# Kernel optimization log

Hardware: AMD Instinct MI355X
Metric: run time of the kernel (lower is better)

The kernel has to match this reference:

```python
import jax, jax.numpy as jnp
import numpy as np

N = 50000
E = 800000
IN_DIM = 512
H1 = IN_DIM // 2   # 256
H2 = IN_DIM // 4   # 128
D = 8
NP_CAYLEY = D * (D - 1) // 2  # 28


def setup_inputs() -> dict:
    key = jax.random.key(0)
    ks = jax.random.split(key, 10)
    x = jax.random.normal(ks[0], (N, IN_DIM), dtype=jnp.float32)
    edge_index = jax.random.randint(ks[1], (2, E), 0, N, dtype=jnp.int64)
    s1 = 1.0 / np.sqrt(IN_DIM)
    s2 = 1.0 / np.sqrt(H1)
    s3 = 1.0 / np.sqrt(H2)
    W1l = jax.random.uniform(ks[2], (H1, IN_DIM), jnp.float32, -s1, s1)
    b1 = jax.random.uniform(ks[3], (H1,), jnp.float32, -s1, s1)
    W1r = jax.random.uniform(ks[4], (H1, IN_DIM), jnp.float32, -s1, s1)
    W2l = jax.random.uniform(ks[5], (H2, H1), jnp.float32, -s2, s2)
    b2 = jax.random.uniform(ks[6], (H2,), jnp.float32, -s2, s2)
    W2r = jax.random.uniform(ks[7], (H2, H1), jnp.float32, -s2, s2)
    Wp = jax.random.uniform(ks[8], (NP_CAYLEY, H2), jnp.float32, -s3, s3)
    bp = jax.random.uniform(ks[9], (NP_CAYLEY,), jnp.float32, -s3, s3)
    return {"x": x, "edge_index": edge_index,
            "W1l": W1l, "b1": b1, "W1r": W1r,
            "W2l": W2l, "b2": b2, "W2r": W2r,
            "Wp": Wp, "bp": bp}


def _sage_conv(x, src, dst, Wl, bl, Wr):
    # PyG SAGEConv (mean aggr): out = lin_l(mean_{j in N(i)} x_j) + lin_r(x_i)
    msg_sum = jax.ops.segment_sum(x[src], dst, num_segments=N)  # [N, F]
    deg = jax.ops.segment_sum(jnp.ones((src.shape[0],), x.dtype), dst,
                              num_segments=N)
    mean = msg_sum / jnp.maximum(deg, 1.0)[:, None]
    return mean @ Wl.T + bl + x @ Wr.T


def _cayley(params):
    # params: [N, d(d-1)/2] -> skew A, then O = (I - A)^{-1} (I + A)
    iu, ju = jnp.triu_indices(D, k=1)  # row-major i<j matches torch loop order
    n = params.shape[0]
    A = jnp.zeros((n, D, D), params.dtype)
    A = A.at[:, iu, ju].set(params)
    A = A.at[:, ju, iu].set(-params)
    I = jnp.eye(D, dtype=params.dtype)
    return jnp.linalg.solve(I[None] - A, I[None] + A)


def reference(x, edge_index, W1l, b1, W1r, W2l, b2, W2r, Wp, bp):
    src, dst = edge_index[0], edge_index[1]
    h = jax.nn.relu(_sage_conv(x, src, dst, W1l, b1, W1r))
    h = jax.nn.relu(_sage_conv(h, src, dst, W2l, b2, W2r))
    params = h @ Wp.T + bp  # [N, 28]
    return _cayley(params)  # [N, 8, 8]
```

## Files before the change

### kernel.cpp

```cpp
#include <hip/hip_runtime.h>
#include <hip/hip_bf16.h>


#define WS_ALIGN(x) (((x) + 255) & ~size_t(255))

typedef __attribute__((ext_vector_type(8))) short short8;
typedef __attribute__((ext_vector_type(4))) float floatx4;

static __device__ __forceinline__ ushort f2b(float f) {
    unsigned u = __builtin_bit_cast(unsigned, f);
    u = (u + 0x7fffu + ((u >> 16) & 1u)) >> 16;
    return (ushort)u;
}
static __device__ __forceinline__ float b2f(ushort h) {
    unsigned u = ((unsigned)h) << 16;
    return __builtin_bit_cast(float, u);
}
static __device__ __forceinline__ unsigned pk2(float a, float b) {
    return (unsigned)f2b(a) | ((unsigned)f2b(b) << 16);
}


__global__ __launch_bounds__(256)
void prep_kernel(const int* __restrict__ dst, int* __restrict__ deg, int E, int eb,
                 const float* __restrict__ W1l, const float* __restrict__ W1r,
                 const float* __restrict__ W2l, const float* __restrict__ W2r,
                 ushort* __restrict__ Wc1, ushort* __restrict__ Wc2) {
    const int b = blockIdx.x;
    const int tid = threadIdx.x;
    if (b < eb) {
        int e = b * 256 + tid;
        if (e < E) atomicAdd(&deg[dst[e]], 1);
    } else {
        int idx = (b - eb) * 256 + tid;
        const int n1 = (512 * 512) / 8;
        const int n2 = (256 * 256) / 8;
        const float* src;
        ushort* dstp;
        if (idx < n1) {
            int e = idx * 8;
            int row = e >> 9, col = e & 511;
            src = (row < 256) ? &W1l[row * 512 + col] : &W1r[(row - 256) * 512 + col];
            dstp = &Wc1[e];
        } else if (idx < n1 + n2) {
            int e = (idx - n1) * 8;
            int row = e >> 8, col = e & 255;
            src = (row < 128) ? &W2l[row * 256 + col] : &W2r[(row - 128) * 256 + col];
            dstp = &Wc2[e];
        } else {
            return;
        }
        const float4* s4 = reinterpret_cast<const float4*>(src);
        float4 v0 = s4[0], v1 = s4[1];
        short8 o;
        o[0] = (short)f2b(v0.x); o[1] = (short)f2b(v0.y);
        o[2] = (short)f2b(v0.z); o[3] = (short)f2b(v0.w);
        o[4] = (short)f2b(v1.x); o[5] = (short)f2b(v1.y);
        o[6] = (short)f2b(v1.z); o[7] = (short)f2b(v1.w);
        *reinterpret_cast<short8*>(dstp) = o;
    }
}


__global__ __launch_bounds__(256)
void scan_phase1(const int* __restrict__ deg, int* __restrict__ bsum, int n) {
    __shared__ int red[256];
    const int t = threadIdx.x;
    const int i = blockIdx.x * 1024 + t * 4;
    int s = 0;
    if (i + 4 <= n) {
        int4 v = *reinterpret_cast<const int4*>(&deg[i]);
        s = v.x + v.y + v.z + v.w;
    } else {
        for (int k = i; k < n; ++k) s += deg[k];
    }
    red[t] = s;
    __syncthreads();
#pragma unroll
    for (int off = 128; off > 0; off >>= 1) {
        if (t < off) red[t] += red[t + off];
        __syncthreads();
    }
    if (t == 0) bsum[blockIdx.x] = red[0];
}

__global__ __launch_bounds__(256)
void scan_phase2(int* __restrict__ bsum, int* __restrict__ rowptr, int nb, int n) {
    __shared__ int sh[256];
    const int t = threadIdx.x;
    int orig = (t < nb) ? bsum[t] : 0;
    sh[t] = orig;
    __syncthreads();
#pragma unroll
    for (int off = 1; off < 256; off <<= 1) {
        int v = (t >= off) ? sh[t - off] : 0;
        __syncthreads();
        sh[t] += v;
        __syncthreads();
    }
    if (t < nb) bsum[t] = sh[t] - orig;
    if (t == 255) rowptr[n] = sh[255];
}

__global__ __launch_bounds__(256)
void scan_phase3(const int* __restrict__ deg, const int* __restrict__ bsum,
                 int* __restrict__ rowptr, int* __restrict__ cursor, int n) {
    __shared__ int red[256];
    const int t = threadIdx.x;
    const int i = blockIdx.x * 1024 + t * 4;
    int v0 = 0, v1 = 0, v2 = 0, v3 = 0;
    if (i + 4 <= n) {
        int4 v = *reinterpret_cast<const int4*>(&deg[i]);
        v0 = v.x; v1 = v.y; v2 = v.z; v3 = v.w;
    } else {
        if (i     < n) v0 = deg[i];
        if (i + 1 < n) v1 = deg[i + 1];
        if (i + 2 < n) v2 = deg[i + 2];
        if (i + 3 < n) v3 = deg[i + 3];
    }
    int s = v0 + v1 + v2 + v3;
    red[t] = s;
    __syncthreads();
#pragma unroll
    for (int off = 1; off < 256; off <<= 1) {
        int u = (t >= off) ? red[t - off] : 0;
        __syncthreads();
        red[t] += u;
        __syncthreads();
    }
    int pre = bsum[blockIdx.x] + red[t] - s;
    if (i + 4 <= n) {
        int4 o;
        o.x = pre; o.y = pre + v0; o.z = pre + v0 + v1; o.w = pre + v0 + v1 + v2;
        *reinterpret_cast<int4*>(&rowptr[i]) = o;
        *reinterpret_cast<int4*>(&cursor[i]) = make_int4(0, 0, 0, 0);
    } else {
        if (i     < n) { rowptr[i]     = pre;                cursor[i]     = 0; }
        if (i + 1 < n) { rowptr[i + 1] = pre + v0;           cursor[i + 1] = 0; }
        if (i + 2 < n) { rowptr[i + 2] = pre + v0 + v1;      cursor[i + 2] = 0; }
        if (i + 3 < n) { rowptr[i + 3] = pre + v0 + v1 + v2; cursor[i + 3] = 0; }
    }
}

__global__ void scatter_kernel(const int* __restrict__ src, const int* __restrict__ dst,
                               const int* __restrict__ rowptr, int* __restrict__ cursor,
                               int* __restrict__ adj, int E) {
    int e = blockIdx.x * blockDim.x + threadIdx.x;
    if (e < E) {
        int d = dst[e];
        int p = atomicAdd(&cursor[d], 1);
        adj[rowptr[d] + p] = src[e];
    }
}


template <bool CASTA>
__global__ __launch_bounds__(512, 4)
void gemm_wide(const float* __restrict__ Af, const ushort* __restrict__ Ab,
               const ushort* __restrict__ B,
               ushort* __restrict__ Cl, ushort* __restrict__ Cr,
               int M, int K, int Ncols, int S) {
    __shared__ ushort As[128 * 64];
    __shared__ ushort Bs[256 * 64];
    const int tid  = threadIdx.x;
    const int wave = tid >> 6;
    const int lane = tid & 63;
    const int row0 = blockIdx.y * 128;
    const int col0 = blockIdx.x * 256;
    const int wm = (wave & 1) * 64;
    const int wn = (wave >> 1) * 64;

    floatx4 acc[4][4];
#pragma unroll
    for (int i = 0; i < 4; ++i)
#pragma unroll
        for (int j = 0; j < 4; ++j)
            acc[i][j] = (floatx4){0.f, 0.f, 0.f, 0.f};

    const int rsub = lane >> 3;
    const int ksw  = ((lane & 7) * 16) ^ (rsub << 4);

    const int ar = tid >> 2;
    const int aq = tid & 3;
    int agrow = row0 + ar; if (agrow >= M) agrow = M - 1;
    const float* arow_base = CASTA ? (Af + (size_t)agrow * K + aq * 16) : nullptr;
    char* alds = (char*)As + ar * 128;
    const int arx = (ar & 7) << 4;

    float4 va0, va1, va2, va3;
    if constexpr (CASTA) {
        const float* s0 = arow_base;
        va0 = *reinterpret_cast<const float4*>(s0 + 0);
        va1 = *reinterpret_cast<const float4*>(s0 + 4);
        va2 = *reinterpret_cast<const float4*>(s0 + 8);
        va3 = *reinterpret_cast<const float4*>(s0 + 12);
    }

    for (int k0 = 0; k0 < K; k0 += 64) {
#pragma unroll
        for (int i = 0; i < 4; ++i) {
            int chunk = wave * 4 + i;
            int r = chunk * 8 + rsub;
            int gcol = col0 + r;
            const char* src = (const char*)(B + (size_t)gcol * K + k0) + ksw;
            __builtin_amdgcn_global_load_lds(
                (const __attribute__((address_space(1))) unsigned int*)src,
                (__attribute__((address_space(3))) unsigned int*)(&Bs[chunk * 512]),
                16, 0, 0);
        }
        if constexpr (CASTA) {
            uint4 o0 = make_uint4(pk2(va0.x, va0.y), pk2(va0.z, va0.w),
                                  pk2(va1.x, va1.y), pk2(va1.z, va1.w));
            uint4 o1 = make_uint4(pk2(va2.x, va2.y), pk2(va2.z, va2.w),
                                  pk2(va3.x, va3.y), pk2(va3.z, va3.w));
            int g0 = aq * 2;
            *reinterpret_cast<uint4*>(alds + ((g0 * 16) ^ arx))       = o0;
            *reinterpret_cast<uint4*>(alds + (((g0 + 1) * 16) ^ arx)) = o1;
            if (k0 + 64 < K) {
                const float* s1 = arow_base + k0 + 64;
                va0 = *reinterpret_cast<const float4*>(s1 + 0);
                va1 = *reinterpret_cast<const float4*>(s1 + 4);
                va2 = *reinterpret_cast<const float4*>(s1 + 8);
                va3 = *reinterpret_cast<const float4*>(s1 + 12);
            }
        } else {
#pragma unroll
            for (int i = 0; i < 2; ++i) {
                int chunk = wave * 2 + i;
                int r = chunk * 8 + rsub;
                int grow = row0 + r;
                if (grow >= M) grow = M - 1;
                const char* src = (const char*)(Ab + (size_t)grow * K + k0) + ksw;
                __builtin_amdgcn_global_load_lds(
                    (const __attribute__((address_space(1))) unsigned int*)src,
                    (__attribute__((address_space(3))) unsigned int*)(&As[chunk * 512]),
                    16, 0, 0);
            }
        }
        __syncthreads();

#pragma unroll
        for (int kk = 0; kk < 2; ++kk) {
            short8 af[4], bf[4];
            const int kb = (kk * 64 + ((lane >> 4) << 4)) ^ ((lane & 7) << 4);
#pragma unroll
            for (int im = 0; im < 4; ++im) {
                int r = wm + im * 16 + (lane & 15);
                af[im] = *reinterpret_cast<const short8*>((const char*)As + r * 128 + kb);
            }
#pragma unroll
            for (int in = 0; in < 4; ++in) {
                int r = wn + in * 16 + (lane & 15);
                bf[in] = *reinterpret_cast<const short8*>((const char*)Bs + r * 128 + kb);
            }
#pragma unroll
            for (int im = 0; im < 4; ++im)
#pragma unroll
                for (int in = 0; in < 4; ++in)
                    acc[im][in] = __builtin_amdgcn_mfma_f32_16x16x32_bf16(
                        af[im], bf[in], acc[im][in], 0, 0, 0);
        }
        __syncthreads();
    }

#pragma unroll
    for (int im = 0; im < 4; ++im) {
#pragma unroll
        for (int reg = 0; reg < 4; ++reg) {
            int r = row0 + wm + im * 16 + ((lane >> 4) << 2) + reg;
            if (r < M) {
#pragma unroll
                for (int in = 0; in < 4; ++in) {
                    int g = col0 + wn + in * 16 + (lane & 15);
                    if (g < S) Cl[(size_t)r * S + g] = f2b(acc[im][in][reg]);
                    else       Cr[(size_t)r * S + (g - S)] = f2b(acc[im][in][reg]);
                }
            }
        }
    }
}


template <int LPN>
__global__ __launch_bounds__(256)
void aggregate_bf16(const ushort* __restrict__ Yl, const ushort* __restrict__ Yr,
                    const float* __restrict__ bias,
                    const int* __restrict__ rowptr, const int* __restrict__ adj,
                    ushort* __restrict__ H, int n) {
    constexpr int F = LPN * 8;
    const int grp = threadIdx.x / LPN;
    const int sub = threadIdx.x % LPN;
    const int node = blockIdx.x * (256 / LPN) + grp;
    if (node >= n) return;
    const int c = sub * 8;
    const int start = rowptr[node], end = rowptr[node + 1];

    float acc[8];
#pragma unroll
    for (int v = 0; v < 8; ++v) acc[v] = 0.f;

    int e = start;
    for (; e + 4 <= end; e += 4) {
        int s0 = adj[e + 0], s1 = adj[e + 1], s2 = adj[e + 2], s3 = adj[e + 3];
        short8 r0 = *reinterpret_cast<const short8*>(&Yl[(size_t)s0 * F + c]);
        short8 r1 = *reinterpret_cast<const short8*>(&Yl[(size_t)s1 * F + c]);
        short8 r2 = *reinterpret_cast<const short8*>(&Yl[(size_t)s2 * F + c]);
        short8 r3 = *reinterpret_cast<const short8*>(&Yl[(size_t)s3 * F + c]);
#pragma unroll
        for (int v = 0; v < 8; ++v)
            acc[v] += (b2f((ushort)r0[v]) + b2f((ushort)r1[v])) +
                      (b2f((ushort)r2[v]) + b2f((ushort)r3[v]));
    }
    for (; e < end; ++e) {
        int s = adj[e];
        short8 r = *reinterpret_cast<const short8*>(&Yl[(size_t)s * F + c]);
#pragma unroll
        for (int v = 0; v < 8; ++v) acc[v] += b2f((ushort)r[v]);
    }

    const int d = end - start;
    const float inv = 1.0f / (float)(d > 0 ? d : 1);
    short8 sv = *reinterpret_cast<const short8*>(&Yr[(size_t)node * F + c]);
    float4 bv0 = *reinterpret_cast<const float4*>(&bias[c]);
    float4 bv1 = *reinterpret_cast<const float4*>(&bias[c + 4]);
    float bb[8] = {bv0.x, bv0.y, bv0.z, bv0.w, bv1.x, bv1.y, bv1.z, bv1.w};
    short8 o;
#pragma unroll
    for (int v = 0; v < 8; ++v)
        o[v] = (short)f2b(fmaxf(acc[v] * inv + b2f((ushort)sv[v]) + bb[v], 0.f));
    *reinterpret_cast<short8*>(&H[(size_t)node * F + c]) = o;
}


__global__ __launch_bounds__(256)
void params_kernel(const ushort* __restrict__ H2, const float* __restrict__ Wp,
                   const float* __restrict__ bp, float* __restrict__ P, int n) {
    __shared__ float WpS[32 * 132];
    __shared__ float bpS[32];
    for (int t = threadIdx.x; t < 32 * 132; t += 256) WpS[t] = 0.f;
    if (threadIdx.x < 32) bpS[threadIdx.x] = (threadIdx.x < 28) ? bp[threadIdx.x] : 0.f;
    __syncthreads();
    for (int t = threadIdx.x; t < 28 * 128; t += 256) {
        int r = t >> 7, c = t & 127;
        WpS[r * 132 + c] = Wp[t];
    }
    __syncthreads();

    const int node = blockIdx.x * 32 + (threadIdx.x >> 3);
    const int l = threadIdx.x & 7;
    if (node >= n) return;

    short8 h8[16];
    const short8* hp = reinterpret_cast<const short8*>(&H2[(size_t)node * 128]);
#pragma unroll
    for (int q = 0; q < 16; ++q) h8[q] = hp[q];

    float acc0 = bpS[l], acc1 = bpS[l + 8], acc2 = bpS[l + 16], acc3 = bpS[l + 24];
#pragma unroll
    for (int q = 0; q < 32; ++q) {
        float h0 = b2f((ushort)h8[q >> 1][(q & 1) * 4 + 0]);
        float h1 = b2f((ushort)h8[q >> 1][(q & 1) * 4 + 1]);
        float h2 = b2f((ushort)h8[q >> 1][(q & 1) * 4 + 2]);
        float h3 = b2f((ushort)h8[q >> 1][(q & 1) * 4 + 3]);
        float4 w0 = *reinterpret_cast<const float4*>(&WpS[(l +  0) * 132 + 4 * q]);
        float4 w1 = *reinterpret_cast<const float4*>(&WpS[(l +  8) * 132 + 4 * q]);
        float4 w2 = *reinterpret_cast<const float4*>(&WpS[(l + 16) * 132 + 4 * q]);
        float4 w3 = *reinterpret_cast<const float4*>(&WpS[(l + 24) * 132 + 4 * q]);
        acc0 += h0 * w0.x + h1 * w0.y + h2 * w0.z + h3 * w0.w;
        acc1 += h0 * w1.x + h1 * w1.y + h2 * w1.z + h3 * w1.w;
        acc2 += h0 * w2.x + h1 * w2.y + h2 * w2.z + h3 * w2.w;
        acc3 += h0 * w3.x + h1 * w3.y + h2 * w3.z + h3 * w3.w;
    }
    float* pout = &P[(size_t)node * 32];
    pout[l]      = acc0;
    pout[l + 8]  = acc1;
    pout[l + 16] = acc2;
    pout[l + 24] = acc3;
}


__global__ __launch_bounds__(256)
void cayley_kernel(const float* __restrict__ P, float* __restrict__ Out, int n) {
    int i = blockIdx.x * blockDim.x + threadIdx.x;
    if (i >= n) return;
    float p[28];
    const float4* pp = reinterpret_cast<const float4*>(&P[(size_t)i * 32]);
#pragma unroll
    for (int q = 0; q < 7; ++q) {
        float4 v = pp[q];
        p[4 * q + 0] = v.x; p[4 * q + 1] = v.y;
        p[4 * q + 2] = v.z; p[4 * q + 3] = v.w;
    }

    float M_[8][8], B_[8][8];
#pragma unroll
    for (int r = 0; r < 8; ++r)
#pragma unroll
        for (int c = 0; c < 8; ++c) {
            M_[r][c] = (r == c) ? 1.f : 0.f;
            B_[r][c] = (r == c) ? 1.f : 0.f;
        }
    {
        int idx = 0;
#pragma unroll
        for (int r = 0; r < 8; ++r)
#pragma unroll
            for (int c = r + 1; c < 8; ++c) {
                float a = p[idx++];
                M_[r][c] -= a;  M_[c][r] += a;
                B_[r][c] += a;  B_[c][r] -= a;
            }
    }
#pragma unroll
    for (int col = 0; col < 8; ++col) {
        float inv = 1.0f / M_[col][col];
#pragma unroll
        for (int c = 0; c < 8; ++c) { M_[col][c] *= inv; B_[col][c] *= inv; }
#pragma unroll
        for (int r = 0; r < 8; ++r) {
            if (r == col) continue;
            float f = M_[r][col];
#pragma unroll
            for (int c = 0; c < 8; ++c) {
                M_[r][c] -= f * M_[col][c];
                B_[r][c] -= f * B_[col][c];
            }
        }
    }
    float* out = &Out[(size_t)i * 64];
#pragma unroll
    for (int r = 0; r < 8; ++r) {
        float4 o0 = make_float4(B_[r][0], B_[r][1], B_[r][2], B_[r][3]);
        float4 o1 = make_float4(B_[r][4], B_[r][5], B_[r][6], B_[r][7]);
        *reinterpret_cast<float4*>(&out[r * 8 + 0]) = o0;
        *reinterpret_cast<float4*>(&out[r * 8 + 4]) = o1;
    }
}


extern "C" void kernel_launch(void* const* d_in, const int* in_sizes, int n_in,
                              void* d_out, int out_size, void* d_ws, size_t ws_size,
                              hipStream_t stream) {
    const float* x   = (const float*)d_in[0];
    const int*   ei  = (const int*)d_in[1];
    const float* W1l = (const float*)d_in[2];
    const float* b1  = (const float*)d_in[3];
    const float* W1r = (const float*)d_in[4];
    const float* W2l = (const float*)d_in[5];
    const float* b2  = (const float*)d_in[6];
    const float* W2r = (const float*)d_in[7];
    const float* Wp  = (const float*)d_in[8];
    const float* bp  = (const float*)d_in[9];
    float* out = (float*)d_out;

    const int IN_DIM = 512;
    const int N = in_sizes[0] / IN_DIM;
    const int E = in_sizes[1] / 2;

    char* ws = (char*)d_ws;
    size_t off = 0;
    int* deg      = (int*)(ws + off); off = WS_ALIGN(off + (size_t)N * 4);
    int* rowptr   = (int*)(ws + off); off = WS_ALIGN(off + (size_t)(N + 1) * 4);
    int* cursor   = (int*)(ws + off); off = WS_ALIGN(off + (size_t)N * 4);
    int* bsum     = (int*)(ws + off); off = WS_ALIGN(off + (size_t)256 * 4);
    int* adj      = (int*)(ws + off); off = WS_ALIGN(off + (size_t)E * 4);
    ushort* Yl    = (ushort*)(ws + off); off = WS_ALIGN(off + (size_t)N * 256 * 2);
    ushort* Yr    = (ushort*)(ws + off); off = WS_ALIGN(off + (size_t)N * 256 * 2);
    ushort* h1    = (ushort*)(ws + off); off = WS_ALIGN(off + (size_t)N * 256 * 2);
    ushort* zl    = (ushort*)(ws + off); off = WS_ALIGN(off + (size_t)N * 128 * 2);
    ushort* zr    = (ushort*)(ws + off); off = WS_ALIGN(off + (size_t)N * 128 * 2);
    ushort* Wc1   = (ushort*)(ws + off); off = WS_ALIGN(off + (size_t)512 * 512 * 2);
    ushort* Wc2   = (ushort*)(ws + off); off = WS_ALIGN(off + (size_t)256 * 256 * 2);
    float*  Pp    = (float*)(ws + off);  off = WS_ALIGN(off + (size_t)N * 32 * 4);

    const int* src = ei;
    const int* dst = ei + E;

    hipMemsetAsync(deg, 0, (size_t)N * 4, stream);

    const int eb = (E + 255) / 256;
    const int wb = ((512 * 512 + 256 * 256) / 8 + 255) / 256;
    const int nb = (N + 1023) / 1024;

    prep_kernel<<<eb + wb, 256, 0, stream>>>(
        dst, deg, E, eb, W1l, W1r, W2l, W2r, Wc1, Wc2);
    scan_phase1<<<nb, 256, 0, stream>>>(deg, bsum, N);
    scan_phase2<<<1, 256, 0, stream>>>(bsum, rowptr, nb, N);
    scan_phase3<<<nb, 256, 0, stream>>>(deg, bsum, rowptr, cursor, N);
    scatter_kernel<<<eb, 256, 0, stream>>>(src, dst, rowptr, cursor, adj, E);

    int gm = (N + 127) / 128;

    gemm_wide<true><<<dim3(2, gm), 512, 0, stream>>>(
        x, (const ushort*)nullptr, Wc1, Yl, Yr, N, 512, 512, 256);
    aggregate_bf16<32><<<(N + 7) / 8, 256, 0, stream>>>(Yl, Yr, b1, rowptr, adj, h1, N);

    gemm_wide<false><<<dim3(1, gm), 512, 0, stream>>>(
        (const float*)nullptr, h1, Wc2, zl, zr, N, 256, 256, 128);
    ushort* h2 = Yl;
    aggregate_bf16<16><<<(N + 15) / 16, 256, 0, stream>>>(zl, zr, b2, rowptr, adj, h2, N);

    params_kernel<<<(N + 31) / 32, 256, 0, stream>>>(h2, Wp, bp, Pp, N);
    cayley_kernel<<<(N + 255) / 256, 256, 0, stream>>>(Pp, out, N);
}
```

Measured before the change: 276.6 us.

## Fuse degree histogram into first GEMM, fuse params with Cayley, split second GEMM

```diff
diff --git a/kernel.cpp b/kernel.cpp
--- a/kernel.cpp
+++ b/kernel.cpp
@@ -22,43 +22,35 @@
 
 
 __global__ __launch_bounds__(256)
-void prep_kernel(const int* __restrict__ dst, int* __restrict__ deg, int E, int eb,
-                 const float* __restrict__ W1l, const float* __restrict__ W1r,
+void prep_kernel(const float* __restrict__ W1l, const float* __restrict__ W1r,
                  const float* __restrict__ W2l, const float* __restrict__ W2r,
                  ushort* __restrict__ Wc1, ushort* __restrict__ Wc2) {
-    const int b = blockIdx.x;
-    const int tid = threadIdx.x;
-    if (b < eb) {
-        int e = b * 256 + tid;
-        if (e < E) atomicAdd(&deg[dst[e]], 1);
+    int idx = blockIdx.x * blockDim.x + threadIdx.x;
+    const int n1 = (512 * 512) / 8;
+    const int n2 = (256 * 256) / 8;
+    const float* src;
+    ushort* dstp;
+    if (idx < n1) {
+        int e = idx * 8;
+        int row = e >> 9, col = e & 511;
+        src = (row < 256) ? &W1l[row * 512 + col] : &W1r[(row - 256) * 512 + col];
+        dstp = &Wc1[e];
+    } else if (idx < n1 + n2) {
+        int e = (idx - n1) * 8;
+        int row = e >> 8, col = e & 255;
+        src = (row < 128) ? &W2l[row * 256 + col] : &W2r[(row - 128) * 256 + col];
+        dstp = &Wc2[e];
     } else {
-        int idx = (b - eb) * 256 + tid;
-        const int n1 = (512 * 512) / 8;
-        const int n2 = (256 * 256) / 8;
-        const float* src;
-        ushort* dstp;
-        if (idx < n1) {
-            int e = idx * 8;
-            int row = e >> 9, col = e & 511;
-            src = (row < 256) ? &W1l[row * 512 + col] : &W1r[(row - 256) * 512 + col];
-            dstp = &Wc1[e];
-        } else if (idx < n1 + n2) {
-            int e = (idx - n1) * 8;
-            int row = e >> 8, col = e & 255;
-            src = (row < 128) ? &W2l[row * 256 + col] : &W2r[(row - 128) * 256 + col];
-            dstp = &Wc2[e];
-        } else {
-            return;
-        }
-        const float4* s4 = reinterpret_cast<const float4*>(src);
-        float4 v0 = s4[0], v1 = s4[1];
-        short8 o;
-        o[0] = (short)f2b(v0.x); o[1] = (short)f2b(v0.y);
-        o[2] = (short)f2b(v0.z); o[3] = (short)f2b(v0.w);
-        o[4] = (short)f2b(v1.x); o[5] = (short)f2b(v1.y);
-        o[6] = (short)f2b(v1.z); o[7] = (short)f2b(v1.w);
-        *reinterpret_cast<short8*>(dstp) = o;
-    }
+        return;
+    }
+    const float4* s4 = reinterpret_cast<const float4*>(src);
+    float4 v0 = s4[0], v1 = s4[1];
+    short8 o;
+    o[0] = (short)f2b(v0.x); o[1] = (short)f2b(v0.y);
+    o[2] = (short)f2b(v0.z); o[3] = (short)f2b(v0.w);
+    o[4] = (short)f2b(v1.x); o[5] = (short)f2b(v1.y);
+    o[6] = (short)f2b(v1.z); o[7] = (short)f2b(v1.w);
+    *reinterpret_cast<short8*>(dstp) = o;
 }
 
 
@@ -154,27 +146,37 @@
 }
 
 
-template <bool CASTA>
-__global__ __launch_bounds__(512, 4)
+template <bool CASTA, int BN, bool HIST>
+__global__ __launch_bounds__(512, 6)
 void gemm_wide(const float* __restrict__ Af, const ushort* __restrict__ Ab,
                const ushort* __restrict__ B,
                ushort* __restrict__ Cl, ushort* __restrict__ Cr,
-               int M, int K, int Ncols, int S) {
+               int M, int K, int S, int gmy,
+               const int* __restrict__ hdst, int* __restrict__ hdeg, int hE) {
+    if (HIST) {
+        if (blockIdx.y >= gmy) {
+            int e = ((blockIdx.y - gmy) * gridDim.x + blockIdx.x) * 512 + threadIdx.x;
+            if (e < hE) atomicAdd(&hdeg[hdst[e]], 1);
+            return;
+        }
+    }
+    constexpr int WN = BN / 4;
+    constexpr int NI = BN / 64;
     __shared__ ushort As[128 * 64];
-    __shared__ ushort Bs[256 * 64];
+    __shared__ ushort Bs[BN * 64];
     const int tid  = threadIdx.x;
     const int wave = tid >> 6;
     const int lane = tid & 63;
     const int row0 = blockIdx.y * 128;
-    const int col0 = blockIdx.x * 256;
+    const int col0 = blockIdx.x * BN;
     const int wm = (wave & 1) * 64;
-    const int wn = (wave >> 1) * 64;
-
-    floatx4 acc[4][4];
+    const int wn = (wave >> 1) * WN;
+
+    floatx4 acc[4][NI];
 #pragma unroll
     for (int i = 0; i < 4; ++i)
 #pragma unroll
-        for (int j = 0; j < 4; ++j)
+        for (int j = 0; j < NI; ++j)
             acc[i][j] = (floatx4){0.f, 0.f, 0.f, 0.f};
 
     const int rsub = lane >> 3;
@@ -198,8 +200,8 @@
 
     for (int k0 = 0; k0 < K; k0 += 64) {
 #pragma unroll
-        for (int i = 0; i < 4; ++i) {
-            int chunk = wave * 4 + i;
+        for (int i = 0; i < NI; ++i) {
+            int chunk = wave * NI + i;
             int r = chunk * 8 + rsub;
             int gcol = col0 + r;
             const char* src = (const char*)(B + (size_t)gcol * K + k0) + ksw;
@@ -241,7 +243,7 @@
 
 #pragma unroll
         for (int kk = 0; kk < 2; ++kk) {
-            short8 af[4], bf[4];
+            short8 af[4], bf[NI];
             const int kb = (kk * 64 + ((lane >> 4) << 4)) ^ ((lane & 7) << 4);
 #pragma unroll
             for (int im = 0; im < 4; ++im) {
@@ -249,14 +251,14 @@
                 af[im] = *reinterpret_cast<const short8*>((const char*)As + r * 128 + kb);
             }
 #pragma unroll
-            for (int in = 0; in < 4; ++in) {
+            for (int in = 0; in < NI; ++in) {
                 int r = wn + in * 16 + (lane & 15);
                 bf[in] = *reinterpret_cast<const short8*>((const char*)Bs + r * 128 + kb);
             }
 #pragma unroll
             for (int im = 0; im < 4; ++im)
 #pragma unroll
-                for (int in = 0; in < 4; ++in)
+                for (int in = 0; in < NI; ++in)
                     acc[im][in] = __builtin_amdgcn_mfma_f32_16x16x32_bf16(
                         af[im], bf[in], acc[im][in], 0, 0, 0);
         }
@@ -270,7 +272,7 @@
             int r = row0 + wm + im * 16 + ((lane >> 4) << 2) + reg;
             if (r < M) {
 #pragma unroll
-                for (int in = 0; in < 4; ++in) {
+                for (int in = 0; in < NI; ++in) {
                     int g = col0 + wn + in * 16 + (lane & 15);
                     if (g < S) Cl[(size_t)r * S + g] = f2b(acc[im][in][reg]);
                     else       Cr[(size_t)r * S + (g - S)] = f2b(acc[im][in][reg]);
@@ -333,10 +335,11 @@
 
 
 __global__ __launch_bounds__(256)
-void params_kernel(const ushort* __restrict__ H2, const float* __restrict__ Wp,
-                   const float* __restrict__ bp, float* __restrict__ P, int n) {
+void params_cayley(const ushort* __restrict__ H2, const float* __restrict__ Wp,
+                   const float* __restrict__ bp, float* __restrict__ Out, int n) {
     __shared__ float WpS[32 * 132];
     __shared__ float bpS[32];
+    __shared__ float Pl[32][36];
     for (int t = threadIdx.x; t < 32 * 132; t += 256) WpS[t] = 0.f;
     if (threadIdx.x < 32) bpS[threadIdx.x] = (threadIdx.x < 28) ? bp[threadIdx.x] : 0.f;
     __syncthreads();
@@ -346,94 +349,90 @@
     }
     __syncthreads();
 
-    const int node = blockIdx.x * 32 + (threadIdx.x >> 3);
+    const int g = threadIdx.x >> 3;
     const int l = threadIdx.x & 7;
-    if (node >= n) return;
-
-    short8 h8[16];
-    const short8* hp = reinterpret_cast<const short8*>(&H2[(size_t)node * 128]);
-#pragma unroll
-    for (int q = 0; q < 16; ++q) h8[q] = hp[q];
-
-    float acc0 = bpS[l], acc1 = bpS[l + 8], acc2 = bpS[l + 16], acc3 = bpS[l + 24];
-#pragma unroll
-    for (int q = 0; q < 32; ++q) {
-        float h0 = b2f((ushort)h8[q >> 1][(q & 1) * 4 + 0]);
-        float h1 = b2f((ushort)h8[q >> 1][(q & 1) * 4 + 1]);
-        float h2 = b2f((ushort)h8[q >> 1][(q & 1) * 4 + 2]);
-        float h3 = b2f((ushort)h8[q >> 1][(q & 1) * 4 + 3]);
-        float4 w0 = *reinterpret_cast<const float4*>(&WpS[(l +  0) * 132 + 4 * q]);
-        float4 w1 = *reinterpret_cast<const float4*>(&WpS[(l +  8) * 132 + 4 * q]);
-        float4 w2 = *reinterpret_cast<const float4*>(&WpS[(l + 16) * 132 + 4 * q]);
-        float4 w3 = *reinterpret_cast<const float4*>(&WpS[(l + 24) * 132 + 4 * q]);
-        acc0 += h0 * w0.x + h1 * w0.y + h2 * w0.z + h3 * w0.w;
-        acc1 += h0 * w1.x + h1 * w1.y + h2 * w1.z + h3 * w1.w;
-        acc2 += h0 * w2.x + h1 * w2.y + h2 * w2.z + h3 * w2.w;
-        acc3 += h0 * w3.x + h1 * w3.y + h2 * w3.z + h3 * w3.w;
-    }
-    float* pout = &P[(size_t)node * 32];
-    pout[l]      = acc0;
-    pout[l + 8]  = acc1;
-    pout[l + 16] = acc2;
-    pout[l + 24] = acc3;
-}
-
-
-__global__ __launch_bounds__(256)
-void cayley_kernel(const float* __restrict__ P, float* __restrict__ Out, int n) {
-    int i = blockIdx.x * blockDim.x + threadIdx.x;
-    if (i >= n) return;
-    float p[28];
-    const float4* pp = reinterpret_cast<const float4*>(&P[(size_t)i * 32]);
-#pragma unroll
-    for (int q = 0; q < 7; ++q) {
-        float4 v = pp[q];
-        p[4 * q + 0] = v.x; p[4 * q + 1] = v.y;
-        p[4 * q + 2] = v.z; p[4 * q + 3] = v.w;
-    }
-
-    float M_[8][8], B_[8][8];
-#pragma unroll
-    for (int r = 0; r < 8; ++r)
-#pragma unroll
-        for (int c = 0; c < 8; ++c) {
-            M_[r][c] = (r == c) ? 1.f : 0.f;
-            B_[r][c] = (r == c) ? 1.f : 0.f;
-        }
-    {
-        int idx = 0;
-#pragma unroll
-        for (int r = 0; r < 8; ++r)
-#pragma unroll
-            for (int c = r + 1; c < 8; ++c) {
-                float a = p[idx++];
-                M_[r][c] -= a;  M_[c][r] += a;
-                B_[r][c] += a;  B_[c][r] -= a;
-            }
-    }
-#pragma unroll
-    for (int col = 0; col < 8; ++col) {
-        float inv = 1.0f / M_[col][col];
-#pragma unroll
-        for (int c = 0; c < 8; ++c) { M_[col][c] *= inv; B_[col][c] *= inv; }
-#pragma unroll
-        for (int r = 0; r < 8; ++r) {
-            if (r == col) continue;
-            float f = M_[r][col];
-#pragma unroll
-            for (int c = 0; c < 8; ++c) {
-                M_[r][c] -= f * M_[col][c];
-                B_[r][c] -= f * B_[col][c];
-            }
-        }
-    }
-    float* out = &Out[(size_t)i * 64];
-#pragma unroll
-    for (int r = 0; r < 8; ++r) {
-        float4 o0 = make_float4(B_[r][0], B_[r][1], B_[r][2], B_[r][3]);
-        float4 o1 = make_float4(B_[r][4], B_[r][5], B_[r][6], B_[r][7]);
-        *reinterpret_cast<float4*>(&out[r * 8 + 0]) = o0;
-        *reinterpret_cast<float4*>(&out[r * 8 + 4]) = o1;
+    const int node = blockIdx.x * 32 + g;
+    if (node < n) {
+        short8 h8[16];
+        const short8* hp = reinterpret_cast<const short8*>(&H2[(size_t)node * 128]);
+#pragma unroll
+        for (int q = 0; q < 16; ++q) h8[q] = hp[q];
+
+        float acc0 = bpS[l], acc1 = bpS[l + 8], acc2 = bpS[l + 16], acc3 = bpS[l + 24];
+#pragma unroll
+        for (int q = 0; q < 32; ++q) {
+            float h0 = b2f((ushort)h8[q >> 1][(q & 1) * 4 + 0]);
+            float h1 = b2f((ushort)h8[q >> 1][(q & 1) * 4 + 1]);
+            float h2 = b2f((ushort)h8[q >> 1][(q & 1) * 4 + 2]);
+            float h3 = b2f((ushort)h8[q >> 1][(q & 1) * 4 + 3]);
+            float4 w0 = *reinterpret_cast<const float4*>(&WpS[(l +  0) * 132 + 4 * q]);
+            float4 w1 = *reinterpret_cast<const float4*>(&WpS[(l +  8) * 132 + 4 * q]);
+            float4 w2 = *reinterpret_cast<const float4*>(&WpS[(l + 16) * 132 + 4 * q]);
+            float4 w3 = *reinterpret_cast<const float4*>(&WpS[(l + 24) * 132 + 4 * q]);
+            acc0 += h0 * w0.x + h1 * w0.y + h2 * w0.z + h3 * w0.w;
+            acc1 += h0 * w1.x + h1 * w1.y + h2 * w1.z + h3 * w1.w;
+            acc2 += h0 * w2.x + h1 * w2.y + h2 * w2.z + h3 * w2.w;
+            acc3 += h0 * w3.x + h1 * w3.y + h2 * w3.z + h3 * w3.w;
+        }
+        Pl[g][l]      = acc0;
+        Pl[g][l + 8]  = acc1;
+        Pl[g][l + 16] = acc2;
+        Pl[g][l + 24] = acc3;
+    }
+    __syncthreads();
+
+    const int t = threadIdx.x;
+    if (t < 32) {
+        int nd = blockIdx.x * 32 + t;
+        if (nd < n) {
+            float p[28];
+#pragma unroll
+            for (int j = 0; j < 28; ++j) p[j] = Pl[t][j];
+
+            float M_[8][8], B_[8][8];
+#pragma unroll
+            for (int r = 0; r < 8; ++r)
+#pragma unroll
+                for (int c = 0; c < 8; ++c) {
+                    M_[r][c] = (r == c) ? 1.f : 0.f;
+                    B_[r][c] = (r == c) ? 1.f : 0.f;
+                }
+            {
+                int idx = 0;
+#pragma unroll
+                for (int r = 0; r < 8; ++r)
+#pragma unroll
+                    for (int c = r + 1; c < 8; ++c) {
+                        float a = p[idx++];
+                        M_[r][c] -= a;  M_[c][r] += a;
+                        B_[r][c] += a;  B_[c][r] -= a;
+                    }
+            }
+#pragma unroll
+            for (int col = 0; col < 8; ++col) {
+                float inv = 1.0f / M_[col][col];
+#pragma unroll
+                for (int c = 0; c < 8; ++c) { M_[col][c] *= inv; B_[col][c] *= inv; }
+#pragma unroll
+                for (int r = 0; r < 8; ++r) {
+                    if (r == col) continue;
+                    float f = M_[r][col];
+#pragma unroll
+                    for (int c = 0; c < 8; ++c) {
+                        M_[r][c] -= f * M_[col][c];
+                        B_[r][c] -= f * B_[col][c];
+                    }
+                }
+            }
+            float* out = &Out[(size_t)nd * 64];
+#pragma unroll
+            for (int r = 0; r < 8; ++r) {
+                float4 o0 = make_float4(B_[r][0], B_[r][1], B_[r][2], B_[r][3]);
+                float4 o1 = make_float4(B_[r][4], B_[r][5], B_[r][6], B_[r][7]);
+                *reinterpret_cast<float4*>(&out[r * 8 + 0]) = o0;
+                *reinterpret_cast<float4*>(&out[r * 8 + 4]) = o1;
+            }
+        }
     }
 }
 
@@ -471,7 +470,6 @@
     ushort* zr    = (ushort*)(ws + off); off = WS_ALIGN(off + (size_t)N * 128 * 2);
     ushort* Wc1   = (ushort*)(ws + off); off = WS_ALIGN(off + (size_t)512 * 512 * 2);
     ushort* Wc2   = (ushort*)(ws + off); off = WS_ALIGN(off + (size_t)256 * 256 * 2);
-    float*  Pp    = (float*)(ws + off);  off = WS_ALIGN(off + (size_t)N * 32 * 4);
 
     const int* src = ei;
     const int* dst = ei + E;
@@ -481,25 +479,27 @@
     const int eb = (E + 255) / 256;
     const int wb = ((512 * 512 + 256 * 256) / 8 + 255) / 256;
     const int nb = (N + 1023) / 1024;
-
-    prep_kernel<<<eb + wb, 256, 0, stream>>>(
-        dst, deg, E, eb, W1l, W1r, W2l, W2r, Wc1, Wc2);
+    const int gm = (N + 127) / 128;
+    const int hb = (E + 1023) / 1024;
+
+    prep_kernel<<<wb, 256, 0, stream>>>(W1l, W1r, W2l, W2r, Wc1, Wc2);
+
+    gemm_wide<true, 256, true><<<dim3(2, gm + hb), 512, 0, stream>>>(
+        x, (const ushort*)nullptr, Wc1, Yl, Yr, N, 512, 256, gm, dst, deg, E);
+
     scan_phase1<<<nb, 256, 0, stream>>>(deg, bsum, N);
     scan_phase2<<<1, 256, 0, stream>>>(bsum, rowptr, nb, N);
     scan_phase3<<<nb, 256, 0, stream>>>(deg, bsum, rowptr, cursor, N);
     scatter_kernel<<<eb, 256, 0, stream>>>(src, dst, rowptr, cursor, adj, E);
 
-    int gm = (N + 127) / 128;
-
-    gemm_wide<true><<<dim3(2, gm), 512, 0, stream>>>(
-        x, (const ushort*)nullptr, Wc1, Yl, Yr, N, 512, 512, 256);
     aggregate_bf16<32><<<(N + 7) / 8, 256, 0, stream>>>(Yl, Yr, b1, rowptr, adj, h1, N);
 
-    gemm_wide<false><<<dim3(1, gm), 512, 0, stream>>>(
-        (const float*)nullptr, h1, Wc2, zl, zr, N, 256, 256, 128);
+    gemm_wide<false, 128, false><<<dim3(2, gm), 512, 0, stream>>>(
+        (const float*)nullptr, h1, Wc2, zl, zr, N, 256, 128, gm,
+        (const int*)nullptr, (int*)nullptr, 0);
+
     ushort* h2 = Yl;
     aggregate_bf16<16><<<(N + 15) / 16, 256, 0, stream>>>(zl, zr, b2, rowptr, adj, h2, N);
 
-    params_kernel<<<(N + 31) / 32, 256, 0, stream>>>(h2, Wp, bp, Pp, N);
-    cayley_kernel<<<(N + 255) / 256, 256, 0, stream>>>(Pp, out, N);
-}
+    params_cayley<<<(N + 31) / 32, 256, 0, stream>>>(h2, Wp, bp, out, N);
+}
```

After: 564.5 us. 104% more time.
